# Kernel optimization log

Measured on AMD Instinct MI355X. Metric: run time of the kernel, lower is better.

Reference implementation:

```python
import jax, jax.numpy as jnp
import numpy as np

N, S, F, E, H, O, L, FE = 8, 1024, 64, 512, 8, 64, 6, 4
HD = E // H
FF = FE * E


def setup_inputs() -> dict:
    key = jax.random.key(0)
    ks = iter(jax.random.split(key, 40))
    def rn(shape, s=0.02):
        return jax.random.normal(next(ks), shape, jnp.float32) * s
    return {
        'x': jax.random.normal(next(ks), (N, F, S), jnp.float32),
        'W_first': rn((F, E)), 'b_first': jnp.zeros((E,), jnp.float32),
        'pos_emb': rn((S, E)),
        'Wq': rn((L, HD, HD)), 'bq': jnp.zeros((L, HD), jnp.float32),
        'Wk': rn((L, HD, HD)), 'bk': jnp.zeros((L, HD), jnp.float32),
        'Wv': rn((L, HD, HD)), 'bv': jnp.zeros((L, HD), jnp.float32),
        'Wo': rn((L, E, E)), 'bo': jnp.zeros((L, E), jnp.float32),
        'g1': jnp.ones((L, E), jnp.float32), 'be1': jnp.zeros((L, E), jnp.float32),
        'Wf1': rn((L, E, FF)), 'bf1': jnp.zeros((L, FF), jnp.float32),
        'Wf2': rn((L, FF, E)), 'bf2': jnp.zeros((L, E), jnp.float32),
        'g2': jnp.ones((L, E), jnp.float32), 'be2': jnp.zeros((L, E), jnp.float32),
        'Wfin': rn((E, O)), 'bfin': jnp.zeros((O,), jnp.float32),
    }


def layernorm(x, g, b, eps=1e-5):
    m = jnp.mean(x, axis=-1, keepdims=True)
    v = jnp.mean(jnp.square(x - m), axis=-1, keepdims=True)
    return (x - m) * jax.lax.rsqrt(v + eps) * g + b


def reference(x, W_first, b_first, pos_emb, Wq, bq, Wk, bk, Wv, bv, Wo, bo,
              g1, be1, Wf1, bf1, Wf2, bf2, g2, be2, Wfin, bfin):
    # x: (N, F, S) -> (N, S, F)
    h = jax.nn.relu(jnp.einsum('nfs,fe->nse', x, W_first) + b_first) + pos_emb[None]
    scale = E ** 0.5  # note: module scales by sqrt(embed_size), not sqrt(head_dim)
    for i in range(L):
        t = h.reshape(N, S, H, HD)
        q = jnp.einsum('nshd,de->nshe', t, Wq[i]) + bq[i]
        k = jnp.einsum('nshd,de->nshe', t, Wk[i]) + bk[i]
        v = jnp.einsum('nshd,de->nshe', t, Wv[i]) + bv[i]
        energy = jnp.einsum('nqhd,nkhd->nhqk', q, k)  # (N,H,S,S)
        att = jax.nn.softmax(energy / scale, axis=-1)
        o = jnp.einsum('nhqk,nkhd->nqhd', att, v).reshape(N, S, E)
        o = jnp.einsum('nse,ef->nsf', o, Wo[i]) + bo[i]
        hx = layernorm(o + h, g1[i], be1[i])
        ff = jax.nn.relu(jnp.einsum('nse,ef->nsf', hx, Wf1[i]) + bf1[i])
        ff = jnp.einsum('nsf,fe->nse', ff, Wf2[i]) + bf2[i]
        h = layernorm(ff + hx, g2[i], be2[i])
    # Conv1d kernel_size=1 == pointwise linear over channels; output (N, O, S)
    return jnp.einsum('nse,eo->nos', h, Wfin) + bfin[None, :, None]
```

## Files before the change

### kernel.cpp

```cpp
#include <hip/hip_runtime.h>
#include <hip/hip_bf16.h>
#include <math.h>

#define N_ 8
#define S_ 1024
#define F_ 64
#define E_ 512
#define H_ 8
#define O_ 64
#define L_ 6
#define HD_ 64
#define FF_ 2048
#define SCALE_ 0.044194173824159216f
#define LOG2E_ 1.4426950408889634f
#define QSCALE_ (SCALE_ * LOG2E_)

typedef unsigned short u16;
typedef __attribute__((ext_vector_type(4))) unsigned short u16x4;
typedef __attribute__((ext_vector_type(8))) unsigned short u16x8;
typedef __attribute__((ext_vector_type(8))) short short8;
typedef __attribute__((ext_vector_type(4))) float floatx4;

__device__ __forceinline__ u16 f2b(float f) {
    union { float f; unsigned u; } v; v.f = f;
    unsigned u = v.u;
    unsigned r = (u + 0x7FFFu + ((u >> 16) & 1u)) >> 16;
    return (u16)r;
}
__device__ __forceinline__ u16 f2b_fast(float f) {
    union { float f; unsigned u; } v; v.f = f;
    return (u16)((v.u + 0x8000u) >> 16);
}
__device__ __forceinline__ float b2f(u16 h) {
    union { unsigned u; float f; } v; v.u = ((unsigned)h) << 16;
    return v.f;
}

__device__ __forceinline__ void gload16(const u16* g, u16* l) {
    __builtin_amdgcn_global_load_lds(
        (const __attribute__((address_space(1))) void*)g,
        (__attribute__((address_space(3))) void*)l, 16, 0, 0);
}

__global__ __launch_bounds__(256) void first_mfma(
    const float* __restrict__ x, const u16* __restrict__ wt,
    const float* __restrict__ bf, const float* __restrict__ pe,
    u16* __restrict__ resb)
{
    __shared__ u16 a_s[128][72];
    int t = threadIdx.x;
    int w = t >> 6, lane = t & 63, quad = lane >> 4, c16 = lane & 15;
    int rowhalf = w >> 1, colhalf = w & 1;
    int col0 = blockIdx.x * 128;
    int row0 = blockIdx.y * 128;
    int n = row0 >> 10, s0 = row0 & 1023;

    const float* xb = x + (size_t)n * F_ * S_ + s0;
    #pragma unroll
    for (int i = 0; i < 8; i++) {
        int pos = (t + i * 256) * 4;
        int f = pos >> 7, sl = pos & 127;
        float4 v = *(const float4*)&xb[(size_t)f * S_ + sl];
        a_s[sl + 0][f] = f2b_fast(v.x);
        a_s[sl + 1][f] = f2b_fast(v.y);
        a_s[sl + 2][f] = f2b_fast(v.z);
        a_s[sl + 3][f] = f2b_fast(v.w);
    }
    __syncthreads();

    floatx4 acc[4][4];
    #pragma unroll
    for (int mt = 0; mt < 4; mt++)
        #pragma unroll
        for (int nt = 0; nt < 4; nt++) acc[mt][nt] = (floatx4){0.f, 0.f, 0.f, 0.f};

    #pragma unroll
    for (int ks = 0; ks < 2; ks++) {
        short8 af[4], bfr[4];
        #pragma unroll
        for (int mt = 0; mt < 4; mt++)
            af[mt] = *(const short8*)&a_s[rowhalf * 64 + mt * 16 + c16][ks * 32 + quad * 8];
        #pragma unroll
        for (int nt = 0; nt < 4; nt++)
            bfr[nt] = *(const short8*)&wt[(size_t)(col0 + colhalf * 64 + nt * 16 + c16) * F_
                                          + ks * 32 + quad * 8];
        #pragma unroll
        for (int mt = 0; mt < 4; mt++)
            #pragma unroll
            for (int nt = 0; nt < 4; nt++)
                acc[mt][nt] = __builtin_amdgcn_mfma_f32_16x16x32_bf16(
                    af[mt], bfr[nt], acc[mt][nt], 0, 0, 0);
    }

    #pragma unroll
    for (int nt = 0; nt < 4; nt++) {
        int col = col0 + colhalf * 64 + nt * 16 + c16;
        float bv = bf[col];
        #pragma unroll
        for (int mt = 0; mt < 4; mt++) {
            #pragma unroll
            for (int r = 0; r < 4; r++) {
                size_t row = (size_t)row0 + rowhalf * 64 + mt * 16 + quad * 4 + r;
                int s = (int)(row & 1023);
                float v = fmaxf(acc[mt][nt][r] + bv, 0.f) + pe[(size_t)s * E_ + col];
                resb[row * E_ + col] = f2b_fast(v);
            }
        }
    }
}

__global__ __launch_bounds__(256) void wcast_t(
    const float* __restrict__ W0, u16* __restrict__ Wt0, int K, int Nc)
{
    __shared__ float tile[32][33];
    int t = threadIdx.x;
    int bx = blockIdx.x, by = blockIdx.y;
    const float* W = W0 + (size_t)blockIdx.z * K * Nc;
    u16* Wt = Wt0 + (size_t)blockIdx.z * K * Nc;
    #pragma unroll
    for (int i = 0; i < 4; i++) {
        int q = t + i * 256; int r = q >> 5, c = q & 31;
        tile[r][c] = W[(size_t)(by * 32 + r) * Nc + bx * 32 + c];
    }
    __syncthreads();
    #pragma unroll
    for (int i = 0; i < 4; i++) {
        int q = t + i * 256; int r = q >> 5, c = q & 31;
        Wt[(size_t)(bx * 32 + r) * K + by * 32 + c] = f2b(tile[c][r]);
    }
}

__global__ __launch_bounds__(256) void qkvw_cast(
    const float* __restrict__ Wq, const float* __restrict__ Wk,
    const float* __restrict__ Wv,
    u16* __restrict__ wqt, u16* __restrict__ wkt, u16* __restrict__ wvt)
{
    int l = blockIdx.x;
    int t = threadIdx.x;
    size_t off = (size_t)l * HD_ * HD_;
    #pragma unroll
    for (int i = 0; i < 16; i++) {
        int idx = t + i * 256;
        int e = idx >> 6, d = idx & 63;
        wqt[off + idx] = f2b(Wq[off + d * HD_ + e]);
        wkt[off + idx] = f2b(Wk[off + d * HD_ + e]);
        wvt[off + idx] = f2b(Wv[off + d * HD_ + e]);
    }
}

__global__ __launch_bounds__(256) void qkv_mfma(
    const u16* __restrict__ hb,
    const u16* __restrict__ wqt, const u16* __restrict__ wkt,
    const u16* __restrict__ wvt,
    const float* __restrict__ bq, const float* __restrict__ bk,
    const float* __restrict__ bv,
    u16* __restrict__ qo, u16* __restrict__ ko, u16* __restrict__ vo)
{
    __shared__ u16 a_s[128 * 64];
    int t = threadIdx.x;
    int w = t >> 6, lane = t & 63, quad = lane >> 4, c16 = lane & 15;
    size_t row0 = (size_t)blockIdx.x * 128;

    #pragma unroll
    for (int i = 0; i < 4; i++) {
        int q = t + i * 256; int r = q >> 3, c = q & 7;
        *(u16x8*)&a_s[r * 64 + ((c ^ (r & 7)) * 8)] =
            *(const u16x8*)&hb[(row0 + r) * HD_ + c * 8];
    }
    __syncthreads();

    short8 af[2][2];
    #pragma unroll
    for (int mt = 0; mt < 2; mt++)
        #pragma unroll
        for (int ks = 0; ks < 2; ks++) {
            int r = w * 32 + mt * 16 + c16;
            af[mt][ks] = *(const short8*)&a_s[r * 64 + (((ks * 4 + quad) ^ (r & 7)) * 8)];
        }

    const u16* wts[3] = {wqt, wkt, wvt};
    const float* bs[3] = {bq, bk, bv};
    u16* outs[3] = {qo, ko, vo};

    #pragma unroll
    for (int m = 0; m < 3; m++) {
        short8 bfr[4][2];
        #pragma unroll
        for (int nt = 0; nt < 4; nt++)
            #pragma unroll
            for (int ks = 0; ks < 2; ks++)
                bfr[nt][ks] = *(const short8*)&wts[m][(nt * 16 + c16) * HD_ + ks * 32 + quad * 8];
        floatx4 acc[2][4];
        #pragma unroll
        for (int mt = 0; mt < 2; mt++)
            #pragma unroll
            for (int nt = 0; nt < 4; nt++) acc[mt][nt] = (floatx4){0.f, 0.f, 0.f, 0.f};
        #pragma unroll
        for (int ks = 0; ks < 2; ks++)
            #pragma unroll
            for (int mt = 0; mt < 2; mt++)
                #pragma unroll
                for (int nt = 0; nt < 4; nt++)
                    acc[mt][nt] = __builtin_amdgcn_mfma_f32_16x16x32_bf16(
                        af[mt][ks], bfr[nt][ks], acc[mt][nt], 0, 0, 0);
        float osc = (m == 0) ? QSCALE_ : 1.0f;
        #pragma unroll
        for (int nt = 0; nt < 4; nt++) {
            float bv_ = bs[m][nt * 16 + c16];
            #pragma unroll
            for (int mt = 0; mt < 2; mt++)
                #pragma unroll
                for (int r = 0; r < 4; r++)
                    outs[m][(row0 + w * 32 + mt * 16 + quad * 4 + r) * HD_ + nt * 16 + c16] =
                        f2b_fast((acc[mt][nt][r] + bv_) * osc);
        }
    }
}

__global__ __launch_bounds__(256) void vtrans(
    const u16* __restrict__ vb, u16* __restrict__ vt)
{
    int bid = blockIdx.x;
    int st = bid & 15, hh = (bid >> 4) & 7, n = bid >> 7;
    __shared__ u16 tile[64 * 64];
    int t = threadIdx.x;
    #pragma unroll
    for (int i = 0; i < 2; i++) {
        int q = t + i * 256; int sl = q >> 3, c = q & 7;
        *(u16x8*)&tile[sl * 64 + ((c ^ ((sl >> 3) & 7)) * 8)] =
            *(const u16x8*)&vb[(((size_t)(n * S_ + st * 64 + sl)) * H_ + hh) * 64 + c * 8];
    }
    __syncthreads();
    #pragma unroll
    for (int i = 0; i < 2; i++) {
        int q = t + i * 256; int d = q >> 3, sc = q & 7;
        u16x8 v;
        #pragma unroll
        for (int j = 0; j < 8; j++) {
            int row = sc * 8 + j;
            v[j] = tile[row * 64 + (((d >> 3) ^ (row >> 3)) * 8) + (d & 7)];
        }
        *(u16x8*)&vt[((size_t)(n * H_ + hh) * 64 + d) * (size_t)S_ + st * 64 + sc * 8] = v;
    }
}

__global__ __launch_bounds__(256, 4) void attn_mfma(
    const u16* __restrict__ Q, const u16* __restrict__ K,
    const u16* __restrict__ Vt, u16* __restrict__ O)
{
    int bid0 = blockIdx.x;
    int bid = (bid0 & 7) * 128 + (bid0 >> 3);
    int qt = bid & 15, hh = (bid >> 4) & 7, n = bid >> 7;
    int t = threadIdx.x;
    int w = t >> 6, lane = t & 63, quad = lane >> 4, c16 = lane & 15;

    __shared__ u16 qp_s[64 * 64];
    __shared__ u16 k_s[64 * 64];
    __shared__ u16 vt_s[64 * 64];
    u16* p_s = qp_s + w * 16 * 64;

    const size_t qkbase = (size_t)n * S_ * E_ + hh * 64;
    const size_t vtbase = ((size_t)(n * H_ + hh) * 64) * (size_t)S_;

    #pragma unroll
    for (int i = 0; i < 2; i++) {
        int q = t + i * 256; int r = q >> 3, c = q & 7;
        *(u16x8*)&qp_s[r * 64 + ((c ^ (r & 7)) * 8)] =
            *(const u16x8*)&Q[qkbase + (size_t)(qt * 64 + r) * E_ + c * 8];
    }
    __syncthreads();

    short8 qf[2];
    #pragma unroll
    for (int ks = 0; ks < 2; ks++) {
        int r = w * 16 + c16;
        qf[ks] = *(const short8*)&qp_s[r * 64 + (((ks * 4 + quad) ^ (r & 7)) * 8)];
    }

    const short8 ones = {(short)0x3F80, (short)0x3F80, (short)0x3F80, (short)0x3F80,
                         (short)0x3F80, (short)0x3F80, (short)0x3F80, (short)0x3F80};

    floatx4 oaccT[4];
    floatx4 lacc = (floatx4){0.f, 0.f, 0.f, 0.f};
    #pragma unroll
    for (int mt = 0; mt < 4; mt++) oaccT[mt] = (floatx4){0.f, 0.f, 0.f, 0.f};

    int ar = t >> 3, act = t & 7;
    int acq = act * 8;
    u16x8 pk[2], pv[2];
    #pragma unroll
    for (int i = 0; i < 2; i++) {
        pk[i] = *(const u16x8*)&K[qkbase + (size_t)(ar + i * 32) * E_ + acq];
        pv[i] = *(const u16x8*)&Vt[vtbase + (size_t)(ar + i * 32) * S_ + acq];
    }

    for (int k0 = 0; k0 < S_; k0 += 64) {
        #pragma unroll
        for (int i = 0; i < 2; i++) {
            int r = ar + i * 32;
            int sc = (act ^ (r & 7)) * 8;
            *(u16x8*)&k_s[r * 64 + sc] = pk[i];
            *(u16x8*)&vt_s[r * 64 + sc] = pv[i];
        }
        __syncthreads();
        if (k0 + 64 < S_) {
            #pragma unroll
            for (int i = 0; i < 2; i++) {
                pk[i] = *(const u16x8*)&K[qkbase + (size_t)(k0 + 64 + ar + i * 32) * E_ + acq];
                pv[i] = *(const u16x8*)&Vt[vtbase + (size_t)(ar + i * 32) * S_ + k0 + 64 + acq];
            }
        }

        floatx4 st[4];
        #pragma unroll
        for (int mt = 0; mt < 4; mt++) st[mt] = (floatx4){0.f, 0.f, 0.f, 0.f};
        __builtin_amdgcn_s_setprio(1);
        #pragma unroll
        for (int ks = 0; ks < 2; ks++) {
            short8 kf[4];
            #pragma unroll
            for (int mt = 0; mt < 4; mt++) {
                int r = mt * 16 + c16;
                kf[mt] = *(const short8*)&k_s[r * 64 + (((ks * 4 + quad) ^ (r & 7)) * 8)];
            }
            #pragma unroll
            for (int mt = 0; mt < 4; mt++)
                st[mt] = __builtin_amdgcn_mfma_f32_16x16x32_bf16(
                    kf[mt], qf[ks], st[mt], 0, 0, 0);
        }
        __builtin_amdgcn_s_setprio(0);

        #pragma unroll
        for (int mt = 0; mt < 4; mt++) {
            u16x4 h;
            #pragma unroll
            for (int r = 0; r < 4; r++) h[r] = f2b_fast(exp2f(st[mt][r]));
            *(u16x4*)&p_s[c16 * 64 + (((2 * mt + (quad >> 1)) ^ (c16 & 7)) * 8)
                          + (quad & 1) * 4] = h;
        }

        __builtin_amdgcn_s_setprio(1);
        #pragma unroll
        for (int ks = 0; ks < 2; ks++) {
            short8 pf = *(const short8*)&p_s[c16 * 64 + (((ks * 4 + quad) ^ (c16 & 7)) * 8)];
            short8 vf[4];
            #pragma unroll
            for (int mt = 0; mt < 4; mt++) {
                int r = mt * 16 + c16;
                vf[mt] = *(const short8*)&vt_s[r * 64 + (((ks * 4 + quad) ^ (r & 7)) * 8)];
            }
            lacc = __builtin_amdgcn_mfma_f32_16x16x32_bf16(ones, pf, lacc, 0, 0, 0);
            #pragma unroll
            for (int mt = 0; mt < 4; mt++)
                oaccT[mt] = __builtin_amdgcn_mfma_f32_16x16x32_bf16(
                    vf[mt], pf, oaccT[mt], 0, 0, 0);
        }
        __builtin_amdgcn_s_setprio(0);
        __syncthreads();
    }

    {
        float rl = 1.f / lacc[0];
        int s = qt * 64 + w * 16 + c16;
        size_t base = (size_t)(n * S_ + s) * E_ + hh * 64;
        #pragma unroll
        for (int mt = 0; mt < 4; mt++) {
            u16x4 h;
            #pragma unroll
            for (int r = 0; r < 4; r++) h[r] = f2b_fast(oaccT[mt][r] * rl);
            *(u16x4*)&O[base + mt * 16 + quad * 4] = h;
        }
    }
}

template <int MT, int NT, bool RELU, bool HASRES, bool OUTF32, bool OUTBF16>
__global__ __launch_bounds__(256, 2) void gemm_mfma(
    const u16* __restrict__ A, const u16* __restrict__ Bt,
    const float* __restrict__ bias, const u16* __restrict__ resid,
    float* __restrict__ outf, u16* __restrict__ outb, int M, int Nc, int K)
{
    constexpr int MFR = MT / 32;
    constexpr int NFR = NT / 32;
    constexpr int AI  = MT / 32;
    constexpr int BI  = NT / 32;
    __shared__ u16 a_s[MT * 64];
    __shared__ u16 b_s[NT * 64];

    int t = threadIdx.x;
    int w = t >> 6, lane = t & 63, quad = lane >> 4, c16 = lane & 15;
    int rw = w >> 1, cw = w & 1;

    int gx = gridDim.x;
    int nwg = gx * (int)gridDim.y;
    int lin = (int)blockIdx.y * gx + (int)blockIdx.x;
    int cpx = nwg >> 3;
    int id2 = (lin & 7) * cpx + (lin >> 3);
    int bx = id2 % gx, by = id2 / gx;

    size_t row0 = (size_t)by * MT;
    size_t col0 = (size_t)bx * NT;

    size_t aoff[AI]; int adst[AI];
    #pragma unroll
    for (int i = 0; i < AI; i++) {
        int p = t + i * 256;
        int r = p >> 3;
        int kch = (p & 7) ^ (r & 7);
        aoff[i] = (row0 + r) * (size_t)K + kch * 8;
        adst[i] = w * 512 + i * 2048;
    }
    size_t boff[BI]; int bdst[BI];
    #pragma unroll
    for (int i = 0; i < BI; i++) {
        int p = t + i * 256;
        int r = p >> 3;
        int kch = (p & 7) ^ (r & 7);
        boff[i] = (col0 + r) * (size_t)K + kch * 8;
        bdst[i] = w * 512 + i * 2048;
    }

    floatx4 acc[MFR][NFR];
    #pragma unroll
    for (int mt = 0; mt < MFR; mt++)
        #pragma unroll
        for (int nt = 0; nt < NFR; nt++) acc[mt][nt] = (floatx4){0.f, 0.f, 0.f, 0.f};

    for (int k0 = 0; k0 < K; k0 += 64) {
        #pragma unroll
        for (int i = 0; i < AI; i++) gload16(A + aoff[i] + k0, a_s + adst[i]);
        #pragma unroll
        for (int i = 0; i < BI; i++) gload16(Bt + boff[i] + k0, b_s + bdst[i]);
        __syncthreads();

        #pragma unroll
        for (int ks = 0; ks < 2; ks++) {
            short8 af[MFR], bfr[NFR];
            #pragma unroll
            for (int mt = 0; mt < MFR; mt++) {
                int r = rw * (MT / 2) + mt * 16 + c16;
                af[mt] = *(const short8*)&a_s[r * 64 + (((ks * 4 + quad) ^ (r & 7)) * 8)];
            }
            #pragma unroll
            for (int nt = 0; nt < NFR; nt++) {
                int r = cw * (NT / 2) + nt * 16 + c16;
                bfr[nt] = *(const short8*)&b_s[r * 64 + (((ks * 4 + quad) ^ (r & 7)) * 8)];
            }
            #pragma unroll
            for (int mt = 0; mt < MFR; mt++)
                #pragma unroll
                for (int nt = 0; nt < NFR; nt++)
                    acc[mt][nt] = __builtin_amdgcn_mfma_f32_16x16x32_bf16(
                        af[mt], bfr[nt], acc[mt][nt], 0, 0, 0);
        }
        __syncthreads();
    }

    #pragma unroll
    for (int nt = 0; nt < NFR; nt++) {
        int col = (int)col0 + cw * (NT / 2) + nt * 16 + c16;
        float bv = bias[col];
        #pragma unroll
        for (int mt = 0; mt < MFR; mt++) {
            size_t rowb = row0 + rw * (MT / 2) + mt * 16 + quad * 4;
            #pragma unroll
            for (int r = 0; r < 4; r++) {
                size_t row = rowb + r;
                float v = acc[mt][nt][r] + bv;
                if constexpr (HASRES) v += b2f(resid[row * Nc + col]);
                if constexpr (RELU) v = fmaxf(v, 0.f);
                if constexpr (OUTF32) outf[row * Nc + col] = v;
                if constexpr (OUTBF16) outb[row * Nc + col] = f2b_fast(v);
            }
        }
    }
}

__global__ __launch_bounds__(256) void layernorm_k(
    const float* __restrict__ in, const float* __restrict__ g,
    const float* __restrict__ bb, u16* __restrict__ outb)
{
    int row = blockIdx.x;
    int t = threadIdx.x;
    const float* x = in + (size_t)row * E_;
    float x0 = x[t], x1 = x[t + 256];
    float s = x0 + x1;
    #pragma unroll
    for (int off = 32; off; off >>= 1) s += __shfl_down(s, off, 64);
    __shared__ float red[4];
    int wid = t >> 6, lane = t & 63;
    if (lane == 0) red[wid] = s;
    __syncthreads();
    float m = (red[0] + red[1] + red[2] + red[3]) * (1.f / E_);
    float d0 = x0 - m, d1 = x1 - m;
    float sq = d0 * d0 + d1 * d1;
    #pragma unroll
    for (int off = 32; off; off >>= 1) sq += __shfl_down(sq, off, 64);
    __syncthreads();
    if (lane == 0) red[wid] = sq;
    __syncthreads();
    float var = (red[0] + red[1] + red[2] + red[3]) * (1.f / E_);
    float rstd = rsqrtf(var + 1e-5f);
    outb[(size_t)row * E_ + t] = f2b_fast(d0 * rstd * g[t] + bb[t]);
    outb[(size_t)row * E_ + t + 256] = f2b_fast(d1 * rstd * g[t + 256] + bb[t + 256]);
}

__global__ __launch_bounds__(256) void final_mfma(
    const u16* __restrict__ hb, const u16* __restrict__ wft,
    const float* __restrict__ bfin, float* __restrict__ outp)
{
    __shared__ u16 a_s[64][72];
    int t = threadIdx.x;
    int w = t >> 6, lane = t & 63, quad = lane >> 4, c16 = lane & 15;
    size_t row0 = (size_t)blockIdx.x * 64;

    floatx4 acc[4];
    #pragma unroll
    for (int nt = 0; nt < 4; nt++) acc[nt] = (floatx4){0.f, 0.f, 0.f, 0.f};

    int ar = t >> 3, acq = (t & 7) * 8;
    u16x8 pa[2];
    #pragma unroll
    for (int i = 0; i < 2; i++)
        pa[i] = *(const u16x8*)&hb[(row0 + ar + i * 32) * E_ + acq];

    for (int k0 = 0; k0 < E_; k0 += 64) {
        #pragma unroll
        for (int i = 0; i < 2; i++)
            *(u16x8*)&a_s[ar + i * 32][acq] = pa[i];
        __syncthreads();
        if (k0 + 64 < E_) {
            #pragma unroll
            for (int i = 0; i < 2; i++)
                pa[i] = *(const u16x8*)&hb[(row0 + ar + i * 32) * E_ + k0 + 64 + acq];
        }
        #pragma unroll
        for (int ks = 0; ks < 2; ks++) {
            short8 af = *(const short8*)&a_s[w * 16 + c16][ks * 32 + quad * 8];
            #pragma unroll
            for (int nt = 0; nt < 4; nt++) {
                short8 bf = *(const short8*)&wft[(nt * 16 + c16) * E_ + k0 + ks * 32 + quad * 8];
                acc[nt] = __builtin_amdgcn_mfma_f32_16x16x32_bf16(af, bf, acc[nt], 0, 0, 0);
            }
        }
        __syncthreads();
    }

    #pragma unroll
    for (int nt = 0; nt < 4; nt++) {
        int o = nt * 16 + c16;
        float bv = bfin[o];
        #pragma unroll
        for (int r = 0; r < 4; r++) {
            size_t row = row0 + w * 16 + quad * 4 + r;
            int n = (int)(row >> 10), s = (int)(row & 1023);
            outp[((size_t)(n * O_ + o)) * S_ + s] = acc[nt][r] + bv;
        }
    }
}

extern "C" void kernel_launch(void* const* d_in, const int* in_sizes, int n_in,
                              void* d_out, int out_size, void* d_ws, size_t ws_size,
                              hipStream_t stream)
{
    const float* x       = (const float*)d_in[0];
    const float* W_first = (const float*)d_in[1];
    const float* b_first = (const float*)d_in[2];
    const float* pos_emb = (const float*)d_in[3];
    const float* Wq      = (const float*)d_in[4];
    const float* bq      = (const float*)d_in[5];
    const float* Wk      = (const float*)d_in[6];
    const float* bk      = (const float*)d_in[7];
    const float* Wv      = (const float*)d_in[8];
    const float* bv      = (const float*)d_in[9];
    const float* Wo      = (const float*)d_in[10];
    const float* bo      = (const float*)d_in[11];
    const float* g1      = (const float*)d_in[12];
    const float* be1     = (const float*)d_in[13];
    const float* Wf1     = (const float*)d_in[14];
    const float* bf1     = (const float*)d_in[15];
    const float* Wf2     = (const float*)d_in[16];
    const float* bf2     = (const float*)d_in[17];
    const float* g2      = (const float*)d_in[18];
    const float* be2     = (const float*)d_in[19];
    const float* Wfin    = (const float*)d_in[20];
    const float* bfin    = (const float*)d_in[21];
    float* out = (float*)d_out;

    const size_t M4 = (size_t)N_ * S_ * E_;
    float* t1   = (float*)d_ws;
    u16*   resb = (u16*)(t1 + M4);
    u16*   qb   = resb + M4;
    u16*   kb   = qb + M4;
    u16*   vb   = kb + M4;
    u16*   vt   = vb + M4;
    u16*   ob   = vt + M4;
    u16*   ffb  = qb;
    u16*   wot  = ob + M4;
    u16*   wf1t = wot + (size_t)L_ * E_ * E_;
    u16*   wf2t = wf1t + (size_t)L_ * E_ * FF_;
    u16*   wqt  = wf2t + (size_t)L_ * FF_ * E_;
    u16*   wkt  = wqt + (size_t)L_ * HD_ * HD_;
    u16*   wvt  = wkt + (size_t)L_ * HD_ * HD_;
    u16*   wft  = wvt + (size_t)L_ * HD_ * HD_;
    u16*   w1t  = wft + (size_t)O_ * E_;

    const int rows = N_ * S_;

    qkvw_cast<<<L_, 256, 0, stream>>>(Wq, Wk, Wv, wqt, wkt, wvt);
    wcast_t<<<dim3(E_ / 32, F_ / 32, 1), 256, 0, stream>>>(W_first, w1t, F_, E_);
    wcast_t<<<dim3(E_ / 32, E_ / 32, L_), 256, 0, stream>>>(Wo, wot, E_, E_);
    wcast_t<<<dim3(FF_ / 32, E_ / 32, L_), 256, 0, stream>>>(Wf1, wf1t, E_, FF_);
    wcast_t<<<dim3(E_ / 32, FF_ / 32, L_), 256, 0, stream>>>(Wf2, wf2t, FF_, E_);
    wcast_t<<<dim3(O_ / 32, E_ / 32, 1), 256, 0, stream>>>(Wfin, wft, E_, O_);

    first_mfma<<<dim3(E_ / 128, rows / 128), 256, 0, stream>>>(
        x, w1t, b_first, pos_emb, resb);

    for (int i = 0; i < L_; i++) {
        qkv_mfma<<<512, 256, 0, stream>>>(
            resb, wqt + (size_t)i * HD_ * HD_, wkt + (size_t)i * HD_ * HD_,
            wvt + (size_t)i * HD_ * HD_, bq + i * HD_, bk + i * HD_, bv + i * HD_,
            qb, kb, vb);
        vtrans<<<1024, 256, 0, stream>>>(vb, vt);
        attn_mfma<<<1024, 256, 0, stream>>>(qb, kb, vt, ob);
        gemm_mfma<128, 64, false, true, true, false><<<dim3(E_ / 64, rows / 128), 256, 0, stream>>>(
            ob, wot + (size_t)i * E_ * E_, bo + i * E_, resb, t1, nullptr, rows, E_, E_);
        layernorm_k<<<rows, 256, 0, stream>>>(t1, g1 + i * E_, be1 + i * E_, resb);
        gemm_mfma<128, 128, true, false, false, true><<<dim3(FF_ / 128, rows / 128), 256, 0, stream>>>(
            resb, wf1t + (size_t)i * E_ * FF_, bf1 + i * FF_, nullptr, nullptr, ffb,
            rows, FF_, E_);
        gemm_mfma<128, 64, false, true, true, false><<<dim3(E_ / 64, rows / 128), 256, 0, stream>>>(
            ffb, wf2t + (size_t)i * FF_ * E_, bf2 + i * E_, resb, t1, nullptr,
            rows, E_, FF_);
        layernorm_k<<<rows, 256, 0, stream>>>(t1, g2 + i * E_, be2 + i * E_, resb);
    }

    final_mfma<<<rows / 64, 256, 0, stream>>>(resb, wft, bfin, out);
}
```

Baseline: 1.026 ms.

## Fuse V transpose into QKV kernel and layernorm into output-projection GEMMs

The QKV kernel now writes V directly in transposed per-head layout through shared memory, which removes the separate vtrans launch and its round trip. A new gemm_ln kernel has each block own 32 full rows of width 512, so bias, residual add and layernorm happen in the epilogue. This replaces the Wo and Wf2 GEMMs plus their standalone layernorm kernels and drops the fp32 intermediate buffer. The trade-off is a narrow 32-row tile that reloads the full B panel per block and uses single-buffered loads, which could cut GEMM efficiency. Variance is computed as E[x^2]-m^2, which is less numerically stable than the previous two-pass form.

```diff
diff --git a/kernel.cpp b/kernel.cpp
--- a/kernel.cpp
+++ b/kernel.cpp
@@ -153,8 +153,8 @@
     const u16* __restrict__ wqt, const u16* __restrict__ wkt,
     const u16* __restrict__ wvt,
     const float* __restrict__ bq, const float* __restrict__ bk,
-    const float* __restrict__ bv,
-    u16* __restrict__ qo, u16* __restrict__ ko, u16* __restrict__ vo)
+    const float* __restrict__ bvp,
+    u16* __restrict__ qo, u16* __restrict__ ko, u16* __restrict__ vt)
 {
     __shared__ u16 a_s[128 * 64];
     int t = threadIdx.x;
@@ -178,12 +178,11 @@
             af[mt][ks] = *(const short8*)&a_s[r * 64 + (((ks * 4 + quad) ^ (r & 7)) * 8)];
         }
 
-    const u16* wts[3] = {wqt, wkt, wvt};
-    const float* bs[3] = {bq, bk, bv};
-    u16* outs[3] = {qo, ko, vo};
-
-    #pragma unroll
-    for (int m = 0; m < 3; m++) {
+    const u16* wts[2] = {wqt, wkt};
+    const float* bs[2] = {bq, bk};
+    u16* outs[2] = {qo, ko};
+    #pragma unroll
+    for (int m = 0; m < 2; m++) {
         short8 bfr[4][2];
         #pragma unroll
         for (int nt = 0; nt < 4; nt++)
@@ -215,32 +214,53 @@
                         f2b_fast((acc[mt][nt][r] + bv_) * osc);
         }
     }
-}
-
-__global__ __launch_bounds__(256) void vtrans(
-    const u16* __restrict__ vb, u16* __restrict__ vt)
-{
-    int bid = blockIdx.x;
-    int st = bid & 15, hh = (bid >> 4) & 7, n = bid >> 7;
-    __shared__ u16 tile[64 * 64];
-    int t = threadIdx.x;
-    #pragma unroll
-    for (int i = 0; i < 2; i++) {
-        int q = t + i * 256; int sl = q >> 3, c = q & 7;
-        *(u16x8*)&tile[sl * 64 + ((c ^ ((sl >> 3) & 7)) * 8)] =
-            *(const u16x8*)&vb[(((size_t)(n * S_ + st * 64 + sl)) * H_ + hh) * 64 + c * 8];
-    }
-    __syncthreads();
-    #pragma unroll
-    for (int i = 0; i < 2; i++) {
-        int q = t + i * 256; int d = q >> 3, sc = q & 7;
-        u16x8 v;
-        #pragma unroll
-        for (int j = 0; j < 8; j++) {
-            int row = sc * 8 + j;
-            v[j] = tile[row * 64 + (((d >> 3) ^ (row >> 3)) * 8) + (d & 7)];
-        }
-        *(u16x8*)&vt[((size_t)(n * H_ + hh) * 64 + d) * (size_t)S_ + st * 64 + sc * 8] = v;
+
+    {
+        short8 bfr[4][2];
+        #pragma unroll
+        for (int nt = 0; nt < 4; nt++)
+            #pragma unroll
+            for (int ks = 0; ks < 2; ks++)
+                bfr[nt][ks] = *(const short8*)&wvt[(nt * 16 + c16) * HD_ + ks * 32 + quad * 8];
+        floatx4 acc[2][4];
+        #pragma unroll
+        for (int mt = 0; mt < 2; mt++)
+            #pragma unroll
+            for (int nt = 0; nt < 4; nt++) acc[mt][nt] = (floatx4){0.f, 0.f, 0.f, 0.f};
+        #pragma unroll
+        for (int ks = 0; ks < 2; ks++)
+            #pragma unroll
+            for (int mt = 0; mt < 2; mt++)
+                #pragma unroll
+                for (int nt = 0; nt < 4; nt++)
+                    acc[mt][nt] = __builtin_amdgcn_mfma_f32_16x16x32_bf16(
+                        af[mt][ks], bfr[nt][ks], acc[mt][nt], 0, 0, 0);
+
+        __syncthreads();
+        u16* vt_s = a_s;
+        #pragma unroll
+        for (int nt = 0; nt < 4; nt++) {
+            float bv_ = bvp[nt * 16 + c16];
+            #pragma unroll
+            for (int mt = 0; mt < 2; mt++)
+                #pragma unroll
+                for (int r = 0; r < 4; r++) {
+                    int fr = w * 32 + mt * 16 + quad * 4 + r;
+                    int h = fr & 7, sl = fr >> 3;
+                    vt_s[((h * 64 + nt * 16 + c16) * 16) + sl] =
+                        f2b_fast(acc[mt][nt][r] + bv_);
+                }
+        }
+        __syncthreads();
+        int sflat0 = (int)(row0 >> 3);
+        int n = sflat0 >> 10, sbase = sflat0 & 1023;
+        #pragma unroll
+        for (int i = 0; i < 4; i++) {
+            int u = t + i * 256;
+            int h = u >> 7, rest = u & 127, d = rest >> 1, half = rest & 1;
+            *(u16x8*)&vt[((size_t)((n * 8 + h) * 64 + d)) * (size_t)S_ + sbase + half * 8] =
+                *(u16x8*)&vt_s[(h * 64 + d) * 16 + half * 8];
+        }
     }
 }
 
@@ -371,6 +391,140 @@
             *(u16x4*)&O[base + mt * 16 + quad * 4] = h;
         }
     }
+}
+
+__global__ __launch_bounds__(512, 2) void gemm_ln(
+    const u16* __restrict__ A, const u16* __restrict__ Bt,
+    const float* __restrict__ bias, const u16* __restrict__ resid,
+    const float* __restrict__ g, const float* __restrict__ be,
+    u16* __restrict__ outb, int K)
+{
+    __shared__ u16 b_s[512 * 64];
+    int t = threadIdx.x;
+    int w = t >> 6, lane = t & 63, quad = lane >> 4, c16 = lane & 15;
+    size_t row0 = (size_t)blockIdx.x * 32;
+    int wcol = w * 64;
+
+    int rb0 = t >> 3;
+    int kch = (t & 7) ^ (rb0 & 7);
+    size_t bbase = (size_t)rb0 * K + kch * 8;
+    int bdst = w * 512;
+
+    short8 pa[2][2];
+    #pragma unroll
+    for (int mt = 0; mt < 2; mt++)
+        #pragma unroll
+        for (int ks = 0; ks < 2; ks++)
+            pa[mt][ks] = *(const short8*)&A[(row0 + mt * 16 + c16) * (size_t)K
+                                            + ks * 32 + quad * 8];
+
+    floatx4 acc[2][4];
+    #pragma unroll
+    for (int mt = 0; mt < 2; mt++)
+        #pragma unroll
+        for (int nt = 0; nt < 4; nt++) acc[mt][nt] = (floatx4){0.f, 0.f, 0.f, 0.f};
+
+    for (int k0 = 0; k0 < K; k0 += 64) {
+        #pragma unroll
+        for (int i = 0; i < 8; i++)
+            gload16(Bt + bbase + (size_t)i * 64 * K + k0, b_s + bdst + i * 4096);
+
+        short8 af[2][2];
+        #pragma unroll
+        for (int mt = 0; mt < 2; mt++)
+            #pragma unroll
+            for (int ks = 0; ks < 2; ks++) af[mt][ks] = pa[mt][ks];
+
+        __syncthreads();
+
+        if (k0 + 64 < K) {
+            #pragma unroll
+            for (int mt = 0; mt < 2; mt++)
+                #pragma unroll
+                for (int ks = 0; ks < 2; ks++)
+                    pa[mt][ks] = *(const short8*)&A[(row0 + mt * 16 + c16) * (size_t)K
+                                                    + k0 + 64 + ks * 32 + quad * 8];
+        }
+
+        #pragma unroll
+        for (int ks = 0; ks < 2; ks++) {
+            short8 bfr[4];
+            #pragma unroll
+            for (int nt = 0; nt < 4; nt++) {
+                int r = wcol + nt * 16 + c16;
+                bfr[nt] = *(const short8*)&b_s[r * 64 + (((ks * 4 + quad) ^ (r & 7)) * 8)];
+            }
+            #pragma unroll
+            for (int mt = 0; mt < 2; mt++)
+                #pragma unroll
+                for (int nt = 0; nt < 4; nt++)
+                    acc[mt][nt] = __builtin_amdgcn_mfma_f32_16x16x32_bf16(
+                        af[mt][ks], bfr[nt], acc[mt][nt], 0, 0, 0);
+        }
+        __syncthreads();
+    }
+
+    float bvv[4], gv[4], bev[4];
+    #pragma unroll
+    for (int nt = 0; nt < 4; nt++) {
+        int col = wcol + nt * 16 + c16;
+        bvv[nt] = bias[col]; gv[nt] = g[col]; bev[nt] = be[col];
+    }
+    float rs[2][4], rq[2][4];
+    #pragma unroll
+    for (int mt = 0; mt < 2; mt++)
+        #pragma unroll
+        for (int r = 0; r < 4; r++) {
+            size_t row = row0 + mt * 16 + quad * 4 + r;
+            float s = 0.f, q = 0.f;
+            #pragma unroll
+            for (int nt = 0; nt < 4; nt++) {
+                float v = acc[mt][nt][r] + bvv[nt]
+                        + b2f(resid[row * E_ + wcol + nt * 16 + c16]);
+                acc[mt][nt][r] = v; s += v; q += v * v;
+            }
+            rs[mt][r] = s; rq[mt][r] = q;
+        }
+    #pragma unroll
+    for (int off = 1; off <= 8; off <<= 1)
+        #pragma unroll
+        for (int mt = 0; mt < 2; mt++)
+            #pragma unroll
+            for (int r = 0; r < 4; r++) {
+                rs[mt][r] += __shfl_xor(rs[mt][r], off, 64);
+                rq[mt][r] += __shfl_xor(rq[mt][r], off, 64);
+            }
+    float* red = (float*)b_s;
+    if (c16 == 0) {
+        #pragma unroll
+        for (int mt = 0; mt < 2; mt++)
+            #pragma unroll
+            for (int r = 0; r < 4; r++) {
+                int rl = mt * 16 + quad * 4 + r;
+                red[(rl * 8 + w) * 2 + 0] = rs[mt][r];
+                red[(rl * 8 + w) * 2 + 1] = rq[mt][r];
+            }
+    }
+    __syncthreads();
+    #pragma unroll
+    for (int mt = 0; mt < 2; mt++)
+        #pragma unroll
+        for (int r = 0; r < 4; r++) {
+            int rl = mt * 16 + quad * 4 + r;
+            float sm = 0.f, sq = 0.f;
+            #pragma unroll
+            for (int ww = 0; ww < 8; ww++) {
+                sm += red[(rl * 8 + ww) * 2 + 0];
+                sq += red[(rl * 8 + ww) * 2 + 1];
+            }
+            float m = sm * (1.f / E_);
+            float rstd = rsqrtf(sq * (1.f / E_) - m * m + 1e-5f);
+            size_t row = row0 + rl;
+            #pragma unroll
+            for (int nt = 0; nt < 4; nt++)
+                outb[row * E_ + wcol + nt * 16 + c16] =
+                    f2b_fast((acc[mt][nt][r] - m) * rstd * gv[nt] + bev[nt]);
+        }
 }
 
 template <int MT, int NT, bool RELU, bool HASRES, bool OUTF32, bool OUTBF16>
@@ -405,8 +559,8 @@
     for (int i = 0; i < AI; i++) {
         int p = t + i * 256;
         int r = p >> 3;
-        int kch = (p & 7) ^ (r & 7);
-        aoff[i] = (row0 + r) * (size_t)K + kch * 8;
+        int kc = (p & 7) ^ (r & 7);
+        aoff[i] = (row0 + r) * (size_t)K + kc * 8;
         adst[i] = w * 512 + i * 2048;
     }
     size_t boff[BI]; int bdst[BI];
@@ -414,8 +568,8 @@
     for (int i = 0; i < BI; i++) {
         int p = t + i * 256;
         int r = p >> 3;
-        int kch = (p & 7) ^ (r & 7);
-        boff[i] = (col0 + r) * (size_t)K + kch * 8;
+        int kc = (p & 7) ^ (r & 7);
+        boff[i] = (col0 + r) * (size_t)K + kc * 8;
         bdst[i] = w * 512 + i * 2048;
     }
 
@@ -473,35 +627,6 @@
             }
         }
     }
-}
-
-__global__ __launch_bounds__(256) void layernorm_k(
-    const float* __restrict__ in, const float* __restrict__ g,
-    const float* __restrict__ bb, u16* __restrict__ outb)
-{
-    int row = blockIdx.x;
-    int t = threadIdx.x;
-    const float* x = in + (size_t)row * E_;
-    float x0 = x[t], x1 = x[t + 256];
-    float s = x0 + x1;
-    #pragma unroll
-    for (int off = 32; off; off >>= 1) s += __shfl_down(s, off, 64);
-    __shared__ float red[4];
-    int wid = t >> 6, lane = t & 63;
-    if (lane == 0) red[wid] = s;
-    __syncthreads();
-    float m = (red[0] + red[1] + red[2] + red[3]) * (1.f / E_);
-    float d0 = x0 - m, d1 = x1 - m;
-    float sq = d0 * d0 + d1 * d1;
-    #pragma unroll
-    for (int off = 32; off; off >>= 1) sq += __shfl_down(sq, off, 64);
-    __syncthreads();
-    if (lane == 0) red[wid] = sq;
-    __syncthreads();
-    float var = (red[0] + red[1] + red[2] + red[3]) * (1.f / E_);
-    float rstd = rsqrtf(var + 1e-5f);
-    outb[(size_t)row * E_ + t] = f2b_fast(d0 * rstd * g[t] + bb[t]);
-    outb[(size_t)row * E_ + t + 256] = f2b_fast(d1 * rstd * g[t + 256] + bb[t + 256]);
 }
 
 __global__ __launch_bounds__(256) void final_mfma(
@@ -587,12 +712,10 @@
     float* out = (float*)d_out;
 
     const size_t M4 = (size_t)N_ * S_ * E_;
-    float* t1   = (float*)d_ws;
-    u16*   resb = (u16*)(t1 + M4);
+    u16*   resb = (u16*)d_ws;
     u16*   qb   = resb + M4;
     u16*   kb   = qb + M4;
-    u16*   vb   = kb + M4;
-    u16*   vt   = vb + M4;
+    u16*   vt   = kb + M4;
     u16*   ob   = vt + M4;
     u16*   ffb  = qb;
     u16*   wot  = ob + M4;
@@ -620,19 +743,17 @@
         qkv_mfma<<<512, 256, 0, stream>>>(
             resb, wqt + (size_t)i * HD_ * HD_, wkt + (size_t)i * HD_ * HD_,
             wvt + (size_t)i * HD_ * HD_, bq + i * HD_, bk + i * HD_, bv + i * HD_,
-            qb, kb, vb);
-        vtrans<<<1024, 256, 0, stream>>>(vb, vt);
+            qb, kb, vt);
         attn_mfma<<<1024, 256, 0, stream>>>(qb, kb, vt, ob);
-        gemm_mfma<128, 64, false, true, true, false><<<dim3(E_ / 64, rows / 128), 256, 0, stream>>>(
-            ob, wot + (size_t)i * E_ * E_, bo + i * E_, resb, t1, nullptr, rows, E_, E_);
-        layernorm_k<<<rows, 256, 0, stream>>>(t1, g1 + i * E_, be1 + i * E_, resb);
+        gemm_ln<<<rows / 32, 512, 0, stream>>>(
+            ob, wot + (size_t)i * E_ * E_, bo + i * E_, resb,
+            g1 + i * E_, be1 + i * E_, resb, E_);
         gemm_mfma<128, 128, true, false, false, true><<<dim3(FF_ / 128, rows / 128), 256, 0, stream>>>(
             resb, wf1t + (size_t)i * E_ * FF_, bf1 + i * FF_, nullptr, nullptr, ffb,
             rows, FF_, E_);
-        gemm_mfma<128, 64, false, true, true, false><<<dim3(E_ / 64, rows / 128), 256, 0, stream>>>(
-            ffb, wf2t + (size_t)i * FF_ * E_, bf2 + i * E_, resb, t1, nullptr,
-            rows, E_, FF_);
-        layernorm_k<<<rows, 256, 0, stream>>>(t1, g2 + i * E_, be2 + i * E_, resb);
+        gemm_ln<<<rows / 32, 512, 0, stream>>>(
+            ffb, wf2t + (size_t)i * FF_ * E_, bf2 + i * E_, resb,
+            g2 + i * E_, be2 + i * E_, resb, FF_);
     }
 
     final_mfma<<<rows / 64, 256, 0, stream>>>(resb, wft, bfin, out);
```

Measured after the change: 1.057 ms. 3.0% more time.

## Fuse V transpose into QKV kernel, double-buffer attention K/V tiles, merge weight casts

Applied to the files above, without the earlier changes.

The QKV projection kernel now writes V straight out in transposed layout through a shared-memory staging tile, which removes the separate vtrans kernel and its round trip through global memory on every layer. The attention kernel double-buffers the K and V shared tiles so the store of the next tile overlaps compute, leaving one barrier per iteration. The six weight-cast launches are merged into a single wprep launch. The costs are more LDS per attention block, which may reduce occupancy, and an added extra barrier in the QKV kernel.

```diff
diff --git a/kernel.cpp b/kernel.cpp
--- a/kernel.cpp
+++ b/kernel.cpp
@@ -109,14 +109,50 @@
     }
 }
 
-__global__ __launch_bounds__(256) void wcast_t(
-    const float* __restrict__ W0, u16* __restrict__ Wt0, int K, int Nc)
-{
+__global__ __launch_bounds__(256) void wprep(
+    const float* __restrict__ W_first, const float* __restrict__ Wo,
+    const float* __restrict__ Wf1, const float* __restrict__ Wf2,
+    const float* __restrict__ Wfin,
+    const float* __restrict__ Wq, const float* __restrict__ Wk,
+    const float* __restrict__ Wv,
+    u16* __restrict__ w1t, u16* __restrict__ wot, u16* __restrict__ wf1t,
+    u16* __restrict__ wf2t, u16* __restrict__ wft,
+    u16* __restrict__ wqt, u16* __restrict__ wkt, u16* __restrict__ wvt)
+{
+    int b = blockIdx.x;
+    int t = threadIdx.x;
     __shared__ float tile[32][33];
-    int t = threadIdx.x;
-    int bx = blockIdx.x, by = blockIdx.y;
-    const float* W = W0 + (size_t)blockIdx.z * K * Nc;
-    u16* Wt = Wt0 + (size_t)blockIdx.z * K * Nc;
+    const float* W; u16* Wt; int K, Nc, bx, by;
+    if (b < 32) {
+        W = W_first; Wt = w1t; K = F_; Nc = E_; bx = b & 15; by = b >> 4;
+    } else if (b < 32 + 1536) {
+        int i = b - 32; int z = i >> 8; int r = i & 255;
+        W = Wo + (size_t)z * E_ * E_; Wt = wot + (size_t)z * E_ * E_;
+        K = E_; Nc = E_; bx = r & 15; by = r >> 4;
+    } else if (b < 32 + 1536 + 6144) {
+        int i = b - (32 + 1536); int z = i >> 10; int r = i & 1023;
+        W = Wf1 + (size_t)z * E_ * FF_; Wt = wf1t + (size_t)z * E_ * FF_;
+        K = E_; Nc = FF_; bx = r & 63; by = r >> 6;
+    } else if (b < 32 + 1536 + 12288) {
+        int i = b - (32 + 1536 + 6144); int z = i >> 10; int r = i & 1023;
+        W = Wf2 + (size_t)z * FF_ * E_; Wt = wf2t + (size_t)z * FF_ * E_;
+        K = FF_; Nc = E_; bx = r & 15; by = r >> 4;
+    } else if (b < 32 + 1536 + 12288 + 32) {
+        int r = b - (32 + 1536 + 12288);
+        W = Wfin; Wt = wft; K = E_; Nc = O_; bx = r & 1; by = r >> 1;
+    } else {
+        int l = b - (32 + 1536 + 12288 + 32);
+        size_t off = (size_t)l * HD_ * HD_;
+        #pragma unroll
+        for (int i = 0; i < 16; i++) {
+            int idx = t + i * 256;
+            int e = idx >> 6, d = idx & 63;
+            wqt[off + idx] = f2b(Wq[off + d * HD_ + e]);
+            wkt[off + idx] = f2b(Wk[off + d * HD_ + e]);
+            wvt[off + idx] = f2b(Wv[off + d * HD_ + e]);
+        }
+        return;
+    }
     #pragma unroll
     for (int i = 0; i < 4; i++) {
         int q = t + i * 256; int r = q >> 5, c = q & 31;
@@ -127,24 +163,6 @@
     for (int i = 0; i < 4; i++) {
         int q = t + i * 256; int r = q >> 5, c = q & 31;
         Wt[(size_t)(bx * 32 + r) * K + by * 32 + c] = f2b(tile[c][r]);
-    }
-}
-
-__global__ __launch_bounds__(256) void qkvw_cast(
-    const float* __restrict__ Wq, const float* __restrict__ Wk,
-    const float* __restrict__ Wv,
-    u16* __restrict__ wqt, u16* __restrict__ wkt, u16* __restrict__ wvt)
-{
-    int l = blockIdx.x;
-    int t = threadIdx.x;
-    size_t off = (size_t)l * HD_ * HD_;
-    #pragma unroll
-    for (int i = 0; i < 16; i++) {
-        int idx = t + i * 256;
-        int e = idx >> 6, d = idx & 63;
-        wqt[off + idx] = f2b(Wq[off + d * HD_ + e]);
-        wkt[off + idx] = f2b(Wk[off + d * HD_ + e]);
-        wvt[off + idx] = f2b(Wv[off + d * HD_ + e]);
     }
 }
 
@@ -153,8 +171,8 @@
     const u16* __restrict__ wqt, const u16* __restrict__ wkt,
     const u16* __restrict__ wvt,
     const float* __restrict__ bq, const float* __restrict__ bk,
-    const float* __restrict__ bv,
-    u16* __restrict__ qo, u16* __restrict__ ko, u16* __restrict__ vo)
+    const float* __restrict__ bvp,
+    u16* __restrict__ qo, u16* __restrict__ ko, u16* __restrict__ vt)
 {
     __shared__ u16 a_s[128 * 64];
     int t = threadIdx.x;
@@ -178,12 +196,11 @@
             af[mt][ks] = *(const short8*)&a_s[r * 64 + (((ks * 4 + quad) ^ (r & 7)) * 8)];
         }
 
-    const u16* wts[3] = {wqt, wkt, wvt};
-    const float* bs[3] = {bq, bk, bv};
-    u16* outs[3] = {qo, ko, vo};
-
-    #pragma unroll
-    for (int m = 0; m < 3; m++) {
+    const u16* wts[2] = {wqt, wkt};
+    const float* bs[2] = {bq, bk};
+    u16* outs[2] = {qo, ko};
+    #pragma unroll
+    for (int m = 0; m < 2; m++) {
         short8 bfr[4][2];
         #pragma unroll
         for (int nt = 0; nt < 4; nt++)
@@ -215,32 +232,53 @@
                         f2b_fast((acc[mt][nt][r] + bv_) * osc);
         }
     }
-}
-
-__global__ __launch_bounds__(256) void vtrans(
-    const u16* __restrict__ vb, u16* __restrict__ vt)
-{
-    int bid = blockIdx.x;
-    int st = bid & 15, hh = (bid >> 4) & 7, n = bid >> 7;
-    __shared__ u16 tile[64 * 64];
-    int t = threadIdx.x;
-    #pragma unroll
-    for (int i = 0; i < 2; i++) {
-        int q = t + i * 256; int sl = q >> 3, c = q & 7;
-        *(u16x8*)&tile[sl * 64 + ((c ^ ((sl >> 3) & 7)) * 8)] =
-            *(const u16x8*)&vb[(((size_t)(n * S_ + st * 64 + sl)) * H_ + hh) * 64 + c * 8];
-    }
-    __syncthreads();
-    #pragma unroll
-    for (int i = 0; i < 2; i++) {
-        int q = t + i * 256; int d = q >> 3, sc = q & 7;
-        u16x8 v;
-        #pragma unroll
-        for (int j = 0; j < 8; j++) {
-            int row = sc * 8 + j;
-            v[j] = tile[row * 64 + (((d >> 3) ^ (row >> 3)) * 8) + (d & 7)];
-        }
-        *(u16x8*)&vt[((size_t)(n * H_ + hh) * 64 + d) * (size_t)S_ + st * 64 + sc * 8] = v;
+
+    {
+        short8 bfr[4][2];
+        #pragma unroll
+        for (int nt = 0; nt < 4; nt++)
+            #pragma unroll
+            for (int ks = 0; ks < 2; ks++)
+                bfr[nt][ks] = *(const short8*)&wvt[(nt * 16 + c16) * HD_ + ks * 32 + quad * 8];
+        floatx4 acc[2][4];
+        #pragma unroll
+        for (int mt = 0; mt < 2; mt++)
+            #pragma unroll
+            for (int nt = 0; nt < 4; nt++) acc[mt][nt] = (floatx4){0.f, 0.f, 0.f, 0.f};
+        #pragma unroll
+        for (int ks = 0; ks < 2; ks++)
+            #pragma unroll
+            for (int mt = 0; mt < 2; mt++)
+                #pragma unroll
+                for (int nt = 0; nt < 4; nt++)
+                    acc[mt][nt] = __builtin_amdgcn_mfma_f32_16x16x32_bf16(
+                        af[mt][ks], bfr[nt][ks], acc[mt][nt], 0, 0, 0);
+
+        __syncthreads();
+        u16* vt_s = a_s;
+        #pragma unroll
+        for (int nt = 0; nt < 4; nt++) {
+            float bv_ = bvp[nt * 16 + c16];
+            #pragma unroll
+            for (int mt = 0; mt < 2; mt++)
+                #pragma unroll
+                for (int r = 0; r < 4; r++) {
+                    int fr = w * 32 + mt * 16 + quad * 4 + r;
+                    int h = fr & 7, sl = fr >> 3;
+                    vt_s[((h * 64 + nt * 16 + c16) * 16) + sl] =
+                        f2b_fast(acc[mt][nt][r] + bv_);
+                }
+        }
+        __syncthreads();
+        int sflat0 = (int)(row0 >> 3);
+        int n = sflat0 >> 10, sbase = sflat0 & 1023;
+        #pragma unroll
+        for (int i = 0; i < 4; i++) {
+            int u = t + i * 256;
+            int h = u >> 7, rest = u & 127, d = rest >> 1, half = rest & 1;
+            *(u16x8*)&vt[((size_t)((n * 8 + h) * 64 + d)) * (size_t)S_ + sbase + half * 8] =
+                *(u16x8*)&vt_s[(h * 64 + d) * 16 + half * 8];
+        }
     }
 }
 
@@ -255,12 +293,18 @@
     int w = t >> 6, lane = t & 63, quad = lane >> 4, c16 = lane & 15;
 
     __shared__ u16 qp_s[64 * 64];
-    __shared__ u16 k_s[64 * 64];
-    __shared__ u16 vt_s[64 * 64];
+    __shared__ u16 k_s[2][64 * 64];
+    __shared__ u16 vt_s[2][64 * 64];
     u16* p_s = qp_s + w * 16 * 64;
 
     const size_t qkbase = (size_t)n * S_ * E_ + hh * 64;
     const size_t vtbase = ((size_t)(n * H_ + hh) * 64) * (size_t)S_;
+
+    int ar = t >> 3, act = t & 7;
+    int acq = act * 8;
+    int scw[2];
+    #pragma unroll
+    for (int i = 0; i < 2; i++) scw[i] = ((act ^ ((ar + i * 32) & 7)) * 8);
 
     #pragma unroll
     for (int i = 0; i < 2; i++) {
@@ -268,6 +312,12 @@
         *(u16x8*)&qp_s[r * 64 + ((c ^ (r & 7)) * 8)] =
             *(const u16x8*)&Q[qkbase + (size_t)(qt * 64 + r) * E_ + c * 8];
     }
+    u16x8 pk[2], pv[2];
+    #pragma unroll
+    for (int i = 0; i < 2; i++) {
+        pk[i] = *(const u16x8*)&K[qkbase + (size_t)(ar + i * 32) * E_ + acq];
+        pv[i] = *(const u16x8*)&Vt[vtbase + (size_t)(ar + i * 32) * S_ + acq];
+    }
     __syncthreads();
 
     short8 qf[2];
@@ -277,6 +327,14 @@
         qf[ks] = *(const short8*)&qp_s[r * 64 + (((ks * 4 + quad) ^ (r & 7)) * 8)];
     }
 
+    #pragma unroll
+    for (int i = 0; i < 2; i++) {
+        int r = ar + i * 32;
+        *(u16x8*)&k_s[0][r * 64 + scw[i]] = pk[i];
+        *(u16x8*)&vt_s[0][r * 64 + scw[i]] = pv[i];
+    }
+    __syncthreads();
+
     const short8 ones = {(short)0x3F80, (short)0x3F80, (short)0x3F80, (short)0x3F80,
                          (short)0x3F80, (short)0x3F80, (short)0x3F80, (short)0x3F80};
 
@@ -285,25 +343,12 @@
     #pragma unroll
     for (int mt = 0; mt < 4; mt++) oaccT[mt] = (floatx4){0.f, 0.f, 0.f, 0.f};
 
-    int ar = t >> 3, act = t & 7;
-    int acq = act * 8;
-    u16x8 pk[2], pv[2];
-    #pragma unroll
-    for (int i = 0; i < 2; i++) {
-        pk[i] = *(const u16x8*)&K[qkbase + (size_t)(ar + i * 32) * E_ + acq];
-        pv[i] = *(const u16x8*)&Vt[vtbase + (size_t)(ar + i * 32) * S_ + acq];
-    }
-
     for (int k0 = 0; k0 < S_; k0 += 64) {
-        #pragma unroll
-        for (int i = 0; i < 2; i++) {
-            int r = ar + i * 32;
-            int sc = (act ^ (r & 7)) * 8;
-            *(u16x8*)&k_s[r * 64 + sc] = pk[i];
-            *(u16x8*)&vt_s[r * 64 + sc] = pv[i];
-        }
-        __syncthreads();
-        if (k0 + 64 < S_) {
+        int cur = (k0 >> 6) & 1;
+        const u16* ks_ = k_s[cur];
+        const u16* vs_ = vt_s[cur];
+        bool more = (k0 + 64 < S_);
+        if (more) {
             #pragma unroll
             for (int i = 0; i < 2; i++) {
                 pk[i] = *(const u16x8*)&K[qkbase + (size_t)(k0 + 64 + ar + i * 32) * E_ + acq];
@@ -321,7 +366,7 @@
             #pragma unroll
             for (int mt = 0; mt < 4; mt++) {
                 int r = mt * 16 + c16;
-                kf[mt] = *(const short8*)&k_s[r * 64 + (((ks * 4 + quad) ^ (r & 7)) * 8)];
+                kf[mt] = *(const short8*)&ks_[r * 64 + (((ks * 4 + quad) ^ (r & 7)) * 8)];
             }
             #pragma unroll
             for (int mt = 0; mt < 4; mt++)
@@ -347,7 +392,7 @@
             #pragma unroll
             for (int mt = 0; mt < 4; mt++) {
                 int r = mt * 16 + c16;
-                vf[mt] = *(const short8*)&vt_s[r * 64 + (((ks * 4 + quad) ^ (r & 7)) * 8)];
+                vf[mt] = *(const short8*)&vs_[r * 64 + (((ks * 4 + quad) ^ (r & 7)) * 8)];
             }
             lacc = __builtin_amdgcn_mfma_f32_16x16x32_bf16(ones, pf, lacc, 0, 0, 0);
             #pragma unroll
@@ -356,6 +401,17 @@
                     vf[mt], pf, oaccT[mt], 0, 0, 0);
         }
         __builtin_amdgcn_s_setprio(0);
+
+        if (more) {
+            u16* kd = k_s[cur ^ 1];
+            u16* vd = vt_s[cur ^ 1];
+            #pragma unroll
+            for (int i = 0; i < 2; i++) {
+                int r = ar + i * 32;
+                *(u16x8*)&kd[r * 64 + scw[i]] = pk[i];
+                *(u16x8*)&vd[r * 64 + scw[i]] = pv[i];
+            }
+        }
         __syncthreads();
     }
 
@@ -405,8 +461,8 @@
     for (int i = 0; i < AI; i++) {
         int p = t + i * 256;
         int r = p >> 3;
-        int kch = (p & 7) ^ (r & 7);
-        aoff[i] = (row0 + r) * (size_t)K + kch * 8;
+        int kc = (p & 7) ^ (r & 7);
+        aoff[i] = (row0 + r) * (size_t)K + kc * 8;
         adst[i] = w * 512 + i * 2048;
     }
     size_t boff[BI]; int bdst[BI];
@@ -414,8 +470,8 @@
     for (int i = 0; i < BI; i++) {
         int p = t + i * 256;
         int r = p >> 3;
-        int kch = (p & 7) ^ (r & 7);
-        boff[i] = (col0 + r) * (size_t)K + kch * 8;
+        int kc = (p & 7) ^ (r & 7);
+        boff[i] = (col0 + r) * (size_t)K + kc * 8;
         bdst[i] = w * 512 + i * 2048;
     }
 
@@ -591,8 +647,7 @@
     u16*   resb = (u16*)(t1 + M4);
     u16*   qb   = resb + M4;
     u16*   kb   = qb + M4;
-    u16*   vb   = kb + M4;
-    u16*   vt   = vb + M4;
+    u16*   vt   = kb + M4;
     u16*   ob   = vt + M4;
     u16*   ffb  = qb;
     u16*   wot  = ob + M4;
@@ -606,12 +661,9 @@
 
     const int rows = N_ * S_;
 
-    qkvw_cast<<<L_, 256, 0, stream>>>(Wq, Wk, Wv, wqt, wkt, wvt);
-    wcast_t<<<dim3(E_ / 32, F_ / 32, 1), 256, 0, stream>>>(W_first, w1t, F_, E_);
-    wcast_t<<<dim3(E_ / 32, E_ / 32, L_), 256, 0, stream>>>(Wo, wot, E_, E_);
-    wcast_t<<<dim3(FF_ / 32, E_ / 32, L_), 256, 0, stream>>>(Wf1, wf1t, E_, FF_);
-    wcast_t<<<dim3(E_ / 32, FF_ / 32, L_), 256, 0, stream>>>(Wf2, wf2t, FF_, E_);
-    wcast_t<<<dim3(O_ / 32, E_ / 32, 1), 256, 0, stream>>>(Wfin, wft, E_, O_);
+    wprep<<<32 + 1536 + 12288 + 32 + 6, 256, 0, stream>>>(
+        W_first, Wo, Wf1, Wf2, Wfin, Wq, Wk, Wv,
+        w1t, wot, wf1t, wf2t, wft, wqt, wkt, wvt);
 
     first_mfma<<<dim3(E_ / 128, rows / 128), 256, 0, stream>>>(
         x, w1t, b_first, pos_emb, resb);
@@ -620,8 +672,7 @@
         qkv_mfma<<<512, 256, 0, stream>>>(
             resb, wqt + (size_t)i * HD_ * HD_, wkt + (size_t)i * HD_ * HD_,
             wvt + (size_t)i * HD_ * HD_, bq + i * HD_, bk + i * HD_, bv + i * HD_,
-            qb, kb, vb);
-        vtrans<<<1024, 256, 0, stream>>>(vb, vt);
+            qb, kb, vt);
         attn_mfma<<<1024, 256, 0, stream>>>(qb, kb, vt, ob);
         gemm_mfma<128, 64, false, true, true, false><<<dim3(E_ / 64, rows / 128), 256, 0, stream>>>(
             ob, wot + (size_t)i * E_ * E_, bo + i * E_, resb, t1, nullptr, rows, E_, E_);
```

After: 1.005 ms. 2.1% less time.
